# Performance work log

Hardware: AMD Instinct MI355X
Metric: run time of the kernel (lower is better)

The kernel has to match this reference:

```python
import jax, jax.numpy as jnp
import numpy as np
from jax import lax

K = 2000      # node_num of GraphConvolution
H, W = 75, 100  # edge_region_feature spatial grid (from per-pixel concat loops)


def setup_inputs() -> dict:
    key = jax.random.key(0)
    k1, k2, k3, k4 = jax.random.split(key, 4)
    b, c = 8, 512
    edge_region_feature = jax.random.normal(k1, (b, c, H, W), dtype=jnp.float32)
    edge_region_predict = jax.random.normal(k2, (b, 3, H, W), dtype=jnp.float32)
    # GraphConvolution params: kaiming_normal_(fan_out) weights, zero bias
    w1 = jax.random.normal(k3, (512, 128), dtype=jnp.float32) * np.sqrt(2.0 / 128)
    b1 = jnp.zeros((K, 128), dtype=jnp.float32)
    w2 = jax.random.normal(k4, (128, 128), dtype=jnp.float32) * np.sqrt(2.0 / 128)
    b2 = jnp.zeros((K, 128), dtype=jnp.float32)
    return {"edge_region_feature": edge_region_feature,
            "edge_region_predict": edge_region_predict,
            "w1": w1, "b1": b1, "w2": w2, "b2": b2}


def reference(edge_region_feature, edge_region_predict, w1, b1, w2, b2):
    b, c = edge_region_feature.shape[0], edge_region_feature.shape[1]
    # block_feature built as: for x in range(W) for y in range(H) -> node n at (y=n%H, x=n//H)
    block = jnp.transpose(edge_region_feature, (0, 3, 2, 1)).reshape(b, W * H, c)  # (b, 7500, 512)

    # topk over channel-0 prediction, flattened row-major (idx = y*W + x)
    scores = edge_region_predict[:, 0, :, :].reshape(b, -1)            # (b, 7500)
    _vals, topk_idx = lax.top_k(scores, K)
    sorted_idx = jnp.sort(topk_idx, axis=1)                            # (b, 2000) int32

    # gather node features (replicates original's indexing of block_feature)
    node_map = jnp.take_along_axis(block, sorted_idx[:, :, None], axis=1)  # (b, 2000, 512)

    # generate_adjacent_map: decode positions with width=W, connect 8-neighborhood (+self)
    py = sorted_idx // W
    px = sorted_idx % W
    near_y = jnp.abs(py[:, :, None] - py[:, None, :]) <= 1
    near_x = jnp.abs(px[:, :, None] - px[:, None, :]) <= 1
    adj = (near_y & near_x).astype(jnp.float32)                        # (b, 2000, 2000)

    # node_feature_grouping = ReLU6 -> GCN(512->128) -> GCN(128->128)
    inp = jnp.clip(jnp.concatenate([adj, node_map], axis=2), 0.0, 6.0)  # ReLU6 on cat(adj, nodes)
    a = inp[:, :, :K]
    nf = inp[:, :, K:]
    # GCN1: A @ X @ W1 + b1  (in!=out -> no residual)
    x1 = jnp.einsum('bij,bjf->bif', a, nf) @ w1 + b1                   # (b, 2000, 128)
    # GCN2: A @ X1 @ W2 + b2 + X1 (in==out -> residual)
    x2 = jnp.einsum('bij,bjf->bif', a, x1) @ w2 + b2 + x1              # (b, 2000, 128)

    node_output_feature = jnp.tanh(x2)
    return node_output_feature, sorted_idx
```

## Files before the change

kernel.cpp:

```cpp
#include <hip/hip_runtime.h>
#include <cmath>

#define H_DIM 75
#define W_DIM 100
#define HW 7500
#define KSEL 2000
#define BATCH 8
#define CIN 512
#define FDIM 128

__device__ __forceinline__ unsigned int map_key(float f) {
  unsigned int u = __float_as_uint(f);
  return (u & 0x80000000u) ? ~u : (u | 0x80000000u);
}

__device__ __forceinline__ float fast_tanh(float x) {
  float e = __expf(2.0f * x);
  return 1.0f - 2.0f * __builtin_amdgcn_rcpf(e + 1.0f);
}

__global__ __launch_bounds__(1024) void topk_nbr_kernel(
    const float* __restrict__ pred, int* __restrict__ off_ws,
    float* __restrict__ out_idx, unsigned short* __restrict__ nbr,
    unsigned char* __restrict__ cnt)
{
  __shared__ unsigned int keys[HW];
  __shared__ unsigned int hist[256];
  __shared__ unsigned int partials[16];
  __shared__ unsigned int s_prefix, s_kth;
  const int b = blockIdx.x;
  const int tid = threadIdx.x;
  const int lane = tid & 63, w = tid >> 6;
  const float* scores = pred + (size_t)b * 3 * HW;
  for (int i = tid; i < HW; i += 1024) keys[i] = map_key(scores[i]);
  if (tid == 0) { s_prefix = 0u; s_kth = KSEL; }
  __syncthreads();

  for (int shift = 24; shift >= 0; shift -= 8) {
    if (tid < 256) hist[tid] = 0u;
    __syncthreads();
    unsigned int pref = s_prefix;
    unsigned int maskhi = (shift == 24) ? 0u : (0xFFFFFFFFu << (shift + 8));
    for (int i = tid; i < HW; i += 1024) {
      unsigned int k = keys[i];
      if ((k & maskhi) == pref) atomicAdd(&hist[(k >> shift) & 0xFFu], 1u);
    }
    __syncthreads();
    if (tid < 64) {
      unsigned int b0 = hist[tid * 4], b1 = hist[tid * 4 + 1];
      unsigned int b2 = hist[tid * 4 + 2], b3 = hist[tid * 4 + 3];
      unsigned int kth = s_kth;
      unsigned int T = b0 + b1 + b2 + b3;
      #pragma unroll
      for (int off = 1; off < 64; off <<= 1) {
        unsigned int t = __shfl_down(T, off, 64);
        if (tid + off < 64) T += t;
      }
      unsigned int U = __shfl_down(T, 1, 64);
      if (tid == 63) U = 0u;
      unsigned int s3 = b3 + U, s2 = b2 + s3, s1 = b1 + s2, s0 = b0 + s1;
      if (s0 >= kth && s1 < kth) { s_prefix = pref | ((unsigned)(4 * tid + 0) << shift); s_kth = kth - s1; }
      if (s1 >= kth && s2 < kth) { s_prefix = pref | ((unsigned)(4 * tid + 1) << shift); s_kth = kth - s2; }
      if (s2 >= kth && s3 < kth) { s_prefix = pref | ((unsigned)(4 * tid + 2) << shift); s_kth = kth - s3; }
      if (s3 >= kth && U  < kth) { s_prefix = pref | ((unsigned)(4 * tid + 3) << shift); s_kth = kth - U; }
    }
    __syncthreads();
  }
  const unsigned int thresh = s_prefix;

  unsigned int local[8];
  unsigned int sum = 0;
  #pragma unroll
  for (int e = 0; e < 8; ++e) {
    int i = tid * 8 + e;
    unsigned int p = 0;
    if (i < HW) {
      unsigned int ky = keys[i];
      if (ky > thresh) p = 1u;
      else if (ky == thresh) p = (1u << 16);
    }
    local[e] = p; sum += p;
  }
  __syncthreads();
  short* pos_of  = (short*)keys;
  int*   s_idx_sh = (int*)((char*)keys + 15000);
  for (int i = tid; i < HW; i += 1024) pos_of[i] = -1;

  unsigned int inc = sum;
  #pragma unroll
  for (int off = 1; off < 64; off <<= 1) {
    unsigned int t = __shfl_up(inc, off, 64);
    if (lane >= off) inc += t;
  }
  if (lane == 63) partials[w] = inc;
  __syncthreads();
  if (tid < 16) {
    unsigned int v = partials[tid];
    #pragma unroll
    for (int off = 1; off < 16; off <<= 1) {
      unsigned int t = __shfl_up(v, off, 64);
      if (tid >= off) v += t;
    }
    partials[tid] = v;
  }
  __syncthreads();
  unsigned int total = partials[15];
  unsigned int run = (w ? partials[w - 1] : 0u) + inc - sum;
  unsigned int ties = (unsigned int)KSEL - (total & 0xFFFFu);
  #pragma unroll
  for (int e = 0; e < 8; ++e) {
    int i = tid * 8 + e;
    unsigned int p = local[e];
    unsigned int gt_pref = run & 0xFFFFu;
    unsigned int eq_pref = run >> 16;
    bool sel = (p & 1u) || (((p >> 16) != 0u) && eq_pref < ties);
    if (sel) {
      unsigned int pos = gt_pref + (eq_pref < ties ? eq_pref : ties);
      off_ws[b * KSEL + pos] = (i % H_DIM) * W_DIM + i / H_DIM;
      out_idx[b * KSEL + pos] = (float)i;
      s_idx_sh[pos] = i;
      pos_of[i] = (short)pos;
    }
    run += p;
  }
  __syncthreads();

  for (int i = tid; i < KSEL; i += 1024) {
    int q = s_idx_sh[i];
    int py = q / W_DIM, px = q % W_DIM;
    unsigned short tmp[9];
    int c = 0;
    #pragma unroll
    for (int dy = -1; dy <= 1; ++dy) {
      int y = py + dy;
      if ((unsigned)y >= (unsigned)H_DIM) continue;
      #pragma unroll
      for (int dx = -1; dx <= 1; ++dx) {
        int x = px + dx;
        if ((unsigned)x >= (unsigned)W_DIM) continue;
        short p = pos_of[y * W_DIM + x];
        if (p >= 0) tmp[c++] = (unsigned short)p;
      }
    }
    #pragma unroll
    for (int t = 0; t < 9; ++t)
      nbr[(size_t)(b * KSEL + i) * 9 + t] = (t < c) ? tmp[t] : (unsigned short)0;
    cnt[b * KSEL + i] = (unsigned char)c;
  }
}

__global__ __launch_bounds__(512) void gather_kernel(
    const float* __restrict__ feat, const int* __restrict__ off_ws,
    float* __restrict__ NFT)
{
  __shared__ __align__(16) float s_plane[HW];
  const int b = blockIdx.y;
  const int c = blockIdx.x;
  const int tid = threadIdx.x;
  const float4* p4 = (const float4*)(feat + ((size_t)b * CIN + c) * HW);
  float4* sp4 = (float4*)s_plane;
  #pragma unroll
  for (int i = tid; i < HW / 4; i += 512)
    sp4[i] = p4[i];
  __syncthreads();
  if (tid < KSEL / 4) {
    const uint4* o4 = (const uint4*)off_ws + (size_t)b * (KSEL / 4);
    uint4 o = o4[tid];
    float4 v;
    v.x = fminf(fmaxf(s_plane[o.x], 0.f), 6.f);
    v.y = fminf(fmaxf(s_plane[o.y], 0.f), 6.f);
    v.z = fminf(fmaxf(s_plane[o.z], 0.f), 6.f);
    v.w = fminf(fmaxf(s_plane[o.w], 0.f), 6.f);
    float4* orow4 = (float4*)(NFT + ((size_t)b * CIN + c) * KSEL);
    orow4[tid] = v;
  }
}

template<int CDIM, bool CMAJOR>
__global__ __launch_bounds__(256) void gemm_kernel(
    const float* __restrict__ in, const float* __restrict__ wmat,
    float* __restrict__ out)
{
  __shared__ __align__(16) float a_lds[32][36];
  __shared__ __align__(16) float w_lds[32][128];
  const int b = blockIdx.y;
  const int n0 = blockIdx.x * 32;
  const int tid = threadIdx.x;
  const int tf = tid & 31, tr = tid >> 5;
  float acc[4][4] = {{0.f}};
  const float* fb = in + (CMAJOR ? (size_t)b * CIN * KSEL : (size_t)b * KSEL * FDIM);
  for (int cc = 0; cc < CDIM; cc += 32) {
    const float4* w4 = (const float4*)(wmat + cc * 128);
    #pragma unroll
    for (int e = tid; e < 1024; e += 256) {
      int c = e >> 5, f4 = e & 31;
      ((float4*)&w_lds[c][0])[f4] = w4[e];
    }
    if (CMAJOR) {
      int c = tid >> 3, n4 = tid & 7;
      ((float4*)&a_lds[c][0])[n4] =
          *(const float4*)&fb[(size_t)(cc + c) * KSEL + n0 + n4 * 4];
    } else {
      int n = tid >> 3, c4 = tid & 7;
      float4 v = *(const float4*)&fb[(size_t)(n0 + n) * FDIM + cc + c4 * 4];
      a_lds[c4 * 4 + 0][n] = v.x;
      a_lds[c4 * 4 + 1][n] = v.y;
      a_lds[c4 * 4 + 2][n] = v.z;
      a_lds[c4 * 4 + 3][n] = v.w;
    }
    __syncthreads();
    #pragma unroll
    for (int c = 0; c < 32; ++c) {
      float4 av = *(const float4*)&a_lds[c][tr * 4];
      float4 wv = *(const float4*)&w_lds[c][tf * 4];
      acc[0][0] += av.x * wv.x; acc[0][1] += av.x * wv.y; acc[0][2] += av.x * wv.z; acc[0][3] += av.x * wv.w;
      acc[1][0] += av.y * wv.x; acc[1][1] += av.y * wv.y; acc[1][2] += av.y * wv.z; acc[1][3] += av.y * wv.w;
      acc[2][0] += av.z * wv.x; acc[2][1] += av.z * wv.y; acc[2][2] += av.z * wv.z; acc[2][3] += av.z * wv.w;
      acc[3][0] += av.w * wv.x; acc[3][1] += av.w * wv.y; acc[3][2] += av.w * wv.z; acc[3][3] += av.w * wv.w;
    }
    __syncthreads();
  }
  #pragma unroll
  for (int r = 0; r < 4; ++r) {
    int row = n0 + tr * 4 + r;
    if (row < KSEL) {
      float4 v = make_float4(acc[r][0], acc[r][1], acc[r][2], acc[r][3]);
      *(float4*)&out[((size_t)(b * KSEL + row)) * FDIM + tf * 4] = v;
    }
  }
}

__global__ __launch_bounds__(256) void x1_kernel(
    const float* __restrict__ G, const float* __restrict__ b1,
    const unsigned short* __restrict__ nbr, const unsigned char* __restrict__ cnt,
    float* __restrict__ x1)
{
  const int g = threadIdx.x >> 5, lane = threadIdx.x & 31;
  const int node = blockIdx.x * 8 + g;
  const int bb = blockIdx.y;
  const size_t bi = (size_t)bb * KSEL + node;
  const unsigned short* nb = nbr + bi * 9;
  unsigned short idx[9];
  #pragma unroll
  for (int t = 0; t < 9; ++t) idx[t] = nb[t];
  const int c = cnt[bi];
  const float4* G4 = (const float4*)G + (size_t)bb * KSEL * 32;
  float4 v[9];
  #pragma unroll
  for (int t = 0; t < 9; ++t) v[t] = G4[(size_t)idx[t] * 32 + lane];
  float4 acc = ((const float4*)b1)[node * 32 + lane];
  #pragma unroll
  for (int t = 0; t < 9; ++t) {
    float m = (t < c) ? 1.f : 0.f;
    acc.x = fmaf(v[t].x, m, acc.x);
    acc.y = fmaf(v[t].y, m, acc.y);
    acc.z = fmaf(v[t].z, m, acc.z);
    acc.w = fmaf(v[t].w, m, acc.w);
  }
  ((float4*)x1)[bi * 32 + lane] = acc;
}

__global__ __launch_bounds__(256) void out_kernel(
    const float* __restrict__ Hm, const float* __restrict__ x1,
    const float* __restrict__ b2,
    const unsigned short* __restrict__ nbr, const unsigned char* __restrict__ cnt,
    float* __restrict__ out)
{
  const int g = threadIdx.x >> 5, lane = threadIdx.x & 31;
  const int node = blockIdx.x * 8 + g;
  const int bb = blockIdx.y;
  const size_t bi = (size_t)bb * KSEL + node;
  const unsigned short* nb = nbr + bi * 9;
  unsigned short idx[9];
  #pragma unroll
  for (int t = 0; t < 9; ++t) idx[t] = nb[t];
  const int c = cnt[bi];
  const float4* H4 = (const float4*)Hm + (size_t)bb * KSEL * 32;
  float4 v[9];
  #pragma unroll
  for (int t = 0; t < 9; ++t) v[t] = H4[(size_t)idx[t] * 32 + lane];
  float4 acc = ((const float4*)b2)[node * 32 + lane];
  float4 xv = ((const float4*)x1)[bi * 32 + lane];
  acc.x += xv.x; acc.y += xv.y; acc.z += xv.z; acc.w += xv.w;
  #pragma unroll
  for (int t = 0; t < 9; ++t) {
    float m = (t < c) ? 1.f : 0.f;
    acc.x = fmaf(v[t].x, m, acc.x);
    acc.y = fmaf(v[t].y, m, acc.y);
    acc.z = fmaf(v[t].z, m, acc.z);
    acc.w = fmaf(v[t].w, m, acc.w);
  }
  float4 r;
  r.x = fast_tanh(acc.x); r.y = fast_tanh(acc.y);
  r.z = fast_tanh(acc.z); r.w = fast_tanh(acc.w);
  ((float4*)out)[bi * 32 + lane] = r;
}

extern "C" void kernel_launch(void* const* d_in, const int* in_sizes, int n_in,
                              void* d_out, int out_size, void* d_ws, size_t ws_size,
                              hipStream_t stream) {
  const float* feat = (const float*)d_in[0];
  const float* pred = (const float*)d_in[1];
  const float* w1   = (const float*)d_in[2];
  const float* b1   = (const float*)d_in[3];
  const float* w2   = (const float*)d_in[4];
  const float* b2   = (const float*)d_in[5];
  float* out0 = (float*)d_out;
  float* out_idx = out0 + (size_t)BATCH * KSEL * FDIM;

  char* ws = (char*)d_ws;
  int*            off_ws = (int*)(ws + 0);
  unsigned short* nbr    = (unsigned short*)(ws + 64256);
  unsigned char*  cnt    = (unsigned char*)(ws + 352512);
  float*          G      = (float*)(ws + 368640);
  char*           R      = ws + 8560640;
  float*          NFT    = (float*)R;
  float*          x1     = (float*)R;
  float*          Hm     = (float*)(R + 8388608);

  topk_nbr_kernel<<<BATCH, 1024, 0, stream>>>(pred, off_ws, out_idx, nbr, cnt);
  gather_kernel<<<dim3(CIN, BATCH), 512, 0, stream>>>(feat, off_ws, NFT);
  gemm_kernel<CIN, true><<<dim3(63, BATCH), 256, 0, stream>>>(NFT, w1, G);
  x1_kernel<<<dim3(KSEL / 8, BATCH), 256, 0, stream>>>(G, b1, nbr, cnt, x1);
  gemm_kernel<FDIM, false><<<dim3(63, BATCH), 256, 0, stream>>>(x1, w2, Hm);
  out_kernel<<<dim3(KSEL / 8, BATCH), 256, 0, stream>>>(Hm, x1, b2, nbr, cnt, out0);
}
```

Before: 288.5 us.

## Run first GCN projection on bf16x3 MFMA with split hi/lo operands

The gather kernel now emits the clipped node features as bf16 hi/lo pairs, and extra blocks in the top-k kernel pre-transpose and split W1 the same way. The 512->128 projection runs on 32x32x16 bf16 MFMA instructions with three products per step (hi*hi, hi*lo, lo*hi) to approximate fp32 accuracy. The intent is to replace the scalar FP32 FMA GEMM with matrix cores. In exchange, gather writes the same number of bytes as two planes, the A-tile LDS fill uses scalar 2-byte loads, and each K=16 step issues three MFMAs between synchronizations.

After: 268.0 us. -7.1%, faster.

```diff
diff --git a/kernel.cpp b/kernel.cpp
--- a/kernel.cpp
+++ b/kernel.cpp
@@ -9,6 +9,10 @@
 #define CIN 512
 #define FDIM 128
 
+typedef short v4s __attribute__((ext_vector_type(4)));
+typedef short v8s __attribute__((ext_vector_type(8)));
+typedef float v16f __attribute__((ext_vector_type(16)));
+
 __device__ __forceinline__ unsigned int map_key(float f) {
   unsigned int u = __float_as_uint(f);
   return (u & 0x80000000u) ? ~u : (u | 0x80000000u);
@@ -19,17 +23,42 @@
   return 1.0f - 2.0f * __builtin_amdgcn_rcpf(e + 1.0f);
 }
 
+__device__ __forceinline__ unsigned short bf16_rne(float v) {
+  unsigned int u = __float_as_uint(v);
+  unsigned int r = u + 0x7FFFu + ((u >> 16) & 1u);
+  return (unsigned short)(r >> 16);
+}
+__device__ __forceinline__ float bf16_to_f(unsigned short h) {
+  return __uint_as_float(((unsigned int)h) << 16);
+}
+
 __global__ __launch_bounds__(1024) void topk_nbr_kernel(
-    const float* __restrict__ pred, int* __restrict__ off_ws,
-    float* __restrict__ out_idx, unsigned short* __restrict__ nbr,
-    unsigned char* __restrict__ cnt)
+    const float* __restrict__ pred, const float* __restrict__ w1,
+    int* __restrict__ off_ws, float* __restrict__ out_idx,
+    unsigned short* __restrict__ nbr, unsigned char* __restrict__ cnt,
+    unsigned short* __restrict__ w1t_hi, unsigned short* __restrict__ w1t_lo)
 {
   __shared__ unsigned int keys[HW];
   __shared__ unsigned int hist[256];
   __shared__ unsigned int partials[16];
   __shared__ unsigned int s_prefix, s_kth;
+  const int tid = threadIdx.x;
+
+  if (blockIdx.x >= BATCH) {
+    int base = (blockIdx.x - BATCH) * 1024 + tid;
+    #pragma unroll
+    for (int e = base; e < CIN * FDIM; e += 8 * 1024) {
+      int k = e & (CIN - 1), f = e >> 9;
+      float v = w1[k * FDIM + f];
+      unsigned short hi = bf16_rne(v);
+      unsigned short lo = bf16_rne(v - bf16_to_f(hi));
+      w1t_hi[(size_t)f * CIN + k] = hi;
+      w1t_lo[(size_t)f * CIN + k] = lo;
+    }
+    return;
+  }
+
   const int b = blockIdx.x;
-  const int tid = threadIdx.x;
   const int lane = tid & 63, w = tid >> 6;
   const float* scores = pred + (size_t)b * 3 * HW;
   for (int i = tid; i < HW; i += 1024) keys[i] = map_key(scores[i]);
@@ -151,7 +180,7 @@
 
 __global__ __launch_bounds__(512) void gather_kernel(
     const float* __restrict__ feat, const int* __restrict__ off_ws,
-    float* __restrict__ NFT)
+    unsigned short* __restrict__ nft_hi, unsigned short* __restrict__ nft_lo)
 {
   __shared__ __align__(16) float s_plane[HW];
   const int b = blockIdx.y;
@@ -166,18 +195,108 @@
   if (tid < KSEL / 4) {
     const uint4* o4 = (const uint4*)off_ws + (size_t)b * (KSEL / 4);
     uint4 o = o4[tid];
-    float4 v;
-    v.x = fminf(fmaxf(s_plane[o.x], 0.f), 6.f);
-    v.y = fminf(fmaxf(s_plane[o.y], 0.f), 6.f);
-    v.z = fminf(fmaxf(s_plane[o.z], 0.f), 6.f);
-    v.w = fminf(fmaxf(s_plane[o.w], 0.f), 6.f);
-    float4* orow4 = (float4*)(NFT + ((size_t)b * CIN + c) * KSEL);
-    orow4[tid] = v;
-  }
-}
-
-template<int CDIM, bool CMAJOR>
-__global__ __launch_bounds__(256) void gemm_kernel(
+    float v0 = fminf(fmaxf(s_plane[o.x], 0.f), 6.f);
+    float v1 = fminf(fmaxf(s_plane[o.y], 0.f), 6.f);
+    float v2 = fminf(fmaxf(s_plane[o.z], 0.f), 6.f);
+    float v3 = fminf(fmaxf(s_plane[o.w], 0.f), 6.f);
+    ushort4 h, l;
+    h.x = bf16_rne(v0); l.x = bf16_rne(v0 - bf16_to_f(h.x));
+    h.y = bf16_rne(v1); l.y = bf16_rne(v1 - bf16_to_f(h.y));
+    h.z = bf16_rne(v2); l.z = bf16_rne(v2 - bf16_to_f(h.z));
+    h.w = bf16_rne(v3); l.w = bf16_rne(v3 - bf16_to_f(h.w));
+    size_t row = ((size_t)b * CIN + c) * KSEL;
+    ((ushort4*)&nft_hi[row])[tid] = h;
+    ((ushort4*)&nft_lo[row])[tid] = l;
+  }
+}
+
+__global__ __launch_bounds__(256) void gemm1_mfma(
+    const unsigned short* __restrict__ nft_hi,
+    const unsigned short* __restrict__ nft_lo,
+    const unsigned short* __restrict__ w1t_hi,
+    const unsigned short* __restrict__ w1t_lo,
+    float* __restrict__ G)
+{
+  __shared__ unsigned short a_hi[64][20], a_lo[64][20];
+  __shared__ unsigned short b_hi[128][20], b_lo[128][20];
+  const int b = blockIdx.y;
+  const int n0 = blockIdx.x * 64;
+  const int tid = threadIdx.x;
+  const int lane = tid & 63, w = tid >> 6;
+  const int wr = w & 1, wc = w >> 1;
+  const int q = lane >> 5, m = lane & 31;
+  v16f acc0, acc1;
+  #pragma unroll
+  for (int i = 0; i < 16; ++i) { acc0[i] = 0.f; acc1[i] = 0.f; }
+  const unsigned short* nh = nft_hi + (size_t)b * CIN * KSEL;
+  const unsigned short* nl = nft_lo + (size_t)b * CIN * KSEL;
+  const int an = wr * 32 + m;
+  const int f0 = wc * 64 + m;
+
+  for (int k0 = 0; k0 < CIN; k0 += 16) {
+    {
+      int n = tid & 63, ks = (tid >> 6) * 4;
+      #pragma unroll
+      for (int j = 0; j < 4; ++j) {
+        int k = ks + j;
+        size_t gi = (size_t)(k0 + k) * KSEL + n0 + n;
+        a_hi[n][k] = nh[gi];
+        a_lo[n][k] = nl[gi];
+      }
+    }
+    {
+      int f = tid & 127, kh = tid >> 7;
+      const ushort4* sh = (const ushort4*)&w1t_hi[(size_t)f * CIN + k0 + kh * 8];
+      const ushort4* sl = (const ushort4*)&w1t_lo[(size_t)f * CIN + k0 + kh * 8];
+      ushort4 h0 = sh[0], h1 = sh[1], l0 = sl[0], l1 = sl[1];
+      *(ushort4*)&b_hi[f][kh * 8]     = h0;
+      *(ushort4*)&b_hi[f][kh * 8 + 4] = h1;
+      *(ushort4*)&b_lo[f][kh * 8]     = l0;
+      *(ushort4*)&b_lo[f][kh * 8 + 4] = l1;
+    }
+    __syncthreads();
+    v4s ah0 = *(const v4s*)&a_hi[an][q * 8];
+    v4s ah1 = *(const v4s*)&a_hi[an][q * 8 + 4];
+    v4s al0 = *(const v4s*)&a_lo[an][q * 8];
+    v4s al1 = *(const v4s*)&a_lo[an][q * 8 + 4];
+    v8s av_hi = __builtin_shufflevector(ah0, ah1, 0, 1, 2, 3, 4, 5, 6, 7);
+    v8s av_lo = __builtin_shufflevector(al0, al1, 0, 1, 2, 3, 4, 5, 6, 7);
+    {
+      v4s bh0 = *(const v4s*)&b_hi[f0][q * 8];
+      v4s bh1 = *(const v4s*)&b_hi[f0][q * 8 + 4];
+      v4s bl0 = *(const v4s*)&b_lo[f0][q * 8];
+      v4s bl1 = *(const v4s*)&b_lo[f0][q * 8 + 4];
+      v8s bv_hi = __builtin_shufflevector(bh0, bh1, 0, 1, 2, 3, 4, 5, 6, 7);
+      v8s bv_lo = __builtin_shufflevector(bl0, bl1, 0, 1, 2, 3, 4, 5, 6, 7);
+      acc0 = __builtin_amdgcn_mfma_f32_32x32x16_bf16(av_hi, bv_hi, acc0, 0, 0, 0);
+      acc0 = __builtin_amdgcn_mfma_f32_32x32x16_bf16(av_hi, bv_lo, acc0, 0, 0, 0);
+      acc0 = __builtin_amdgcn_mfma_f32_32x32x16_bf16(av_lo, bv_hi, acc0, 0, 0, 0);
+    }
+    {
+      v4s bh0 = *(const v4s*)&b_hi[f0 + 32][q * 8];
+      v4s bh1 = *(const v4s*)&b_hi[f0 + 32][q * 8 + 4];
+      v4s bl0 = *(const v4s*)&b_lo[f0 + 32][q * 8];
+      v4s bl1 = *(const v4s*)&b_lo[f0 + 32][q * 8 + 4];
+      v8s bv_hi = __builtin_shufflevector(bh0, bh1, 0, 1, 2, 3, 4, 5, 6, 7);
+      v8s bv_lo = __builtin_shufflevector(bl0, bl1, 0, 1, 2, 3, 4, 5, 6, 7);
+      acc1 = __builtin_amdgcn_mfma_f32_32x32x16_bf16(av_hi, bv_hi, acc1, 0, 0, 0);
+      acc1 = __builtin_amdgcn_mfma_f32_32x32x16_bf16(av_hi, bv_lo, acc1, 0, 0, 0);
+      acc1 = __builtin_amdgcn_mfma_f32_32x32x16_bf16(av_lo, bv_hi, acc1, 0, 0, 0);
+    }
+    __syncthreads();
+  }
+  float* ob = G + (size_t)b * KSEL * FDIM;
+  #pragma unroll
+  for (int reg = 0; reg < 16; ++reg) {
+    int row = n0 + wr * 32 + (reg & 3) + 8 * (reg >> 2) + 4 * q;
+    if (row < KSEL) {
+      ob[(size_t)row * FDIM + f0]      = acc0[reg];
+      ob[(size_t)row * FDIM + f0 + 32] = acc1[reg];
+    }
+  }
+}
+
+__global__ __launch_bounds__(256) void gemm2_kernel(
     const float* __restrict__ in, const float* __restrict__ wmat,
     float* __restrict__ out)
 {
@@ -188,19 +307,15 @@
   const int tid = threadIdx.x;
   const int tf = tid & 31, tr = tid >> 5;
   float acc[4][4] = {{0.f}};
-  const float* fb = in + (CMAJOR ? (size_t)b * CIN * KSEL : (size_t)b * KSEL * FDIM);
-  for (int cc = 0; cc < CDIM; cc += 32) {
+  const float* fb = in + (size_t)b * KSEL * FDIM;
+  for (int cc = 0; cc < FDIM; cc += 32) {
     const float4* w4 = (const float4*)(wmat + cc * 128);
     #pragma unroll
     for (int e = tid; e < 1024; e += 256) {
       int c = e >> 5, f4 = e & 31;
       ((float4*)&w_lds[c][0])[f4] = w4[e];
     }
-    if (CMAJOR) {
-      int c = tid >> 3, n4 = tid & 7;
-      ((float4*)&a_lds[c][0])[n4] =
-          *(const float4*)&fb[(size_t)(cc + c) * KSEL + n0 + n4 * 4];
-    } else {
+    {
       int n = tid >> 3, c4 = tid & 7;
       float4 v = *(const float4*)&fb[(size_t)(n0 + n) * FDIM + cc + c4 * 4];
       a_lds[c4 * 4 + 0][n] = v.x;
@@ -314,14 +429,18 @@
   unsigned char*  cnt    = (unsigned char*)(ws + 352512);
   float*          G      = (float*)(ws + 368640);
   char*           R      = ws + 8560640;
-  float*          NFT    = (float*)R;
+  unsigned short* nft_hi = (unsigned short*)R;
+  unsigned short* nft_lo = (unsigned short*)(R + 16384000);
+  unsigned short* w1t_hi = (unsigned short*)(R + 32768256);
+  unsigned short* w1t_lo = (unsigned short*)(R + 32899328);
   float*          x1     = (float*)R;
   float*          Hm     = (float*)(R + 8388608);
 
-  topk_nbr_kernel<<<BATCH, 1024, 0, stream>>>(pred, off_ws, out_idx, nbr, cnt);
-  gather_kernel<<<dim3(CIN, BATCH), 512, 0, stream>>>(feat, off_ws, NFT);
-  gemm_kernel<CIN, true><<<dim3(63, BATCH), 256, 0, stream>>>(NFT, w1, G);
+  topk_nbr_kernel<<<BATCH + 8, 1024, 0, stream>>>(pred, w1, off_ws, out_idx,
+                                                  nbr, cnt, w1t_hi, w1t_lo);
+  gather_kernel<<<dim3(CIN, BATCH), 512, 0, stream>>>(feat, off_ws, nft_hi, nft_lo);
+  gemm1_mfma<<<dim3(32, BATCH), 256, 0, stream>>>(nft_hi, nft_lo, w1t_hi, w1t_lo, G);
   x1_kernel<<<dim3(KSEL / 8, BATCH), 256, 0, stream>>>(G, b1, nbr, cnt, x1);
-  gemm_kernel<FDIM, false><<<dim3(63, BATCH), 256, 0, stream>>>(x1, w2, Hm);
+  gemm2_kernel<<<dim3(63, BATCH), 256, 0, stream>>>(x1, w2, Hm);
   out_kernel<<<dim3(KSEL / 8, BATCH), 256, 0, stream>>>(Hm, x1, b2, nbr, cnt, out0);
 }
```
